# Kernel tuning notes

Measured on AMD Instinct MI355X. Metric: run time of the kernel, lower is better.

The kernel has to match this reference:

```python
import jax, jax.numpy as jnp
import numpy as np

B, N, T, CIN = 16, 400, 12, 2
HID, H, D = 256, 8, 32
P, EMB, TOPK, K = 3, 10, 16, 3


def _conv1d(x, w, b, dil):
    # x: (BN, C, T), w: (O, I, K); causal (left) padding like F.pad((pad,0))
    pad = (K - 1) * dil
    y = jax.lax.conv_general_dilated(x, w, (1,), [(pad, 0)], rhs_dilation=(dil,),
                                     dimension_numbers=('NCH', 'OIH', 'NCH'))
    return y + b[None, :, None]


def _ln(x, g, b):
    m = x.mean(-1, keepdims=True)
    v = x.var(-1, keepdims=True)
    return (x - m) / jnp.sqrt(v + 1e-5) * g + b


def setup_inputs() -> dict:
    key = jax.random.key(0)
    kit = iter(jax.random.split(key, 64))

    def g(shape, s=0.05):
        return jax.random.normal(next(kit), shape, jnp.float32) * s

    # fixed graph: ring with 8 neighbors + self loop -> L = 9*N edges
    idx = np.arange(N)
    offs = np.array([-4, -3, -2, -1, 0, 1, 2, 3, 4])
    recv = np.repeat(idx, offs.size)
    send = (recv + np.tile(offs, N)) % N
    L = recv.size

    inp = {
        'x': g((B, N, T, CIN), 1.0),
        'edge_feat': g((B, L, 2), 1.0),
        'fixed_edge_index': jnp.asarray(np.stack([recv, send]).astype(np.int32)),
        # GTCN layer 0 (dilation 1): gate/filter/skip convs + LayerNorm
        'wg0': g((HID, CIN, K)), 'bg0': jnp.zeros((HID,), jnp.float32),
        'wf0': g((HID, CIN, K)), 'bf0': jnp.zeros((HID,), jnp.float32),
        'ws0': g((HID, CIN, K)), 'bs0': jnp.zeros((HID,), jnp.float32),
        'ln0g': jnp.ones((HID,), jnp.float32), 'ln0b': jnp.zeros((HID,), jnp.float32),
        # GTCN layer 1 (dilation 2)
        'wg1': g((HID, HID, K)), 'bg1': jnp.zeros((HID,), jnp.float32),
        'wf1': g((HID, HID, K)), 'bf1': jnp.zeros((HID,), jnp.float32),
        'ws1': g((HID, HID, K)), 'bs1': jnp.zeros((HID,), jnp.float32),
        'ln1g': jnp.ones((HID,), jnp.float32), 'ln1b': jnp.zeros((HID,), jnp.float32),
        'wsk': g((CIN, HID)), 'bsk': jnp.zeros((HID,), jnp.float32),
        # sparse GAT on fixed physical graph (with 2-dim edge features)
        'sWq': g((HID, HID)), 'sWk': g((HID, HID)), 'sWv': g((HID, HID)),
        'sWe': g((2, HID)),
        'saq': g((H, D)), 'sak': g((H, D)), 'sae': g((H, D)),
        # dense GAT on adaptive adjacency
        'dWq': g((HID, HID)), 'dWk': g((HID, HID)), 'dWv': g((HID, HID)),
        'daq': g((H, D)), 'dak': g((H, D)),
        'E1': g((N, EMB), 0.5), 'E2': g((N, EMB), 0.5),
        # gated fusion
        'fW1': g((HID, HID)), 'fb1': jnp.zeros((HID,), jnp.float32),
        'fW2': g((HID, HID)), 'fb2': jnp.zeros((HID,), jnp.float32),
        'fW3': g((HID, HID)), 'fb3': jnp.zeros((HID,), jnp.float32),
        # prediction head
        'Wo': g((HID, P)), 'bo': jnp.zeros((P,), jnp.float32),
    }
    return inp


def reference(x, edge_feat,
              wg0, bg0, wf0, bf0, ws0, bs0, ln0g, ln0b,
              wg1, bg1, wf1, bf1, ws1, bs1, ln1g, ln1b, wsk, bsk,
              sWq, sWk, sWv, sWe, saq, sak, sae,
              dWq, dWk, dWv, daq, dak, E1, E2,
              fW1, fb1, fW2, fb2, fW3, fb3, Wo, bo,
              fixed_edge_index):
    Bb, Nn, Tt, _ = x.shape
    # ---- GTCN (gated temporal conv stack with residual skip) ----
    res = x @ wsk + bsk                                   # (B,N,T,HID)
    xc = x.reshape(Bb * Nn, Tt, -1).transpose(0, 2, 1)    # (BN,C,T)
    for (wg, bg, wf, bf, ws, bs, lg, lb), dil in (
            ((wg0, bg0, wf0, bf0, ws0, bs0, ln0g, ln0b), 1),
            ((wg1, bg1, wf1, bf1, ws1, bs1, ln1g, ln1b), 2)):
        gate = jax.nn.sigmoid(_conv1d(xc, wg, bg, dil))
        y = gate * _conv1d(xc, wf, bf, dil) + (1 - gate) * _conv1d(xc, ws, bs, dil)
        y = jax.nn.relu(_ln(y.transpose(0, 2, 1), lg, lb))  # (BN,T,HID)
        xc = y.transpose(0, 2, 1)
    h = xc.transpose(0, 2, 1).reshape(Bb, Nn, Tt, HID) + res
    hl = h[:, :, -1, :]                                   # (B,N,HID) last step

    # ---- sparse GAT on fixed physical graph (edge features) ----
    recv, send = fixed_edge_index[0], fixed_edge_index[1]
    q = (hl @ sWq).reshape(Bb, Nn, H, D)
    k = (hl @ sWk).reshape(Bb, Nn, H, D)
    v = (hl @ sWv).reshape(Bb, Nn, H, D)
    e = (edge_feat @ sWe).reshape(Bb, -1, H, D)
    s = (q[:, recv] * saq).sum(-1) + (k[:, send] * sak).sum(-1) + (e * sae).sum(-1)
    s = jax.nn.leaky_relu(s, 0.2)                         # (B,L,H)
    mx = jnp.full((Bb, Nn, H), -jnp.inf, s.dtype).at[:, recv].max(s)
    ex = jnp.exp(s - mx[:, recv])
    den = jnp.zeros((Bb, Nn, H), s.dtype).at[:, recv].add(ex)
    alpha = ex / jnp.clip(den[:, recv], 1e-12, None)
    agg = jnp.zeros((Bb, Nn, H, D), v.dtype).at[:, recv].add(alpha[..., None] * v[:, send])
    h_fixed = jax.nn.elu(agg.reshape(Bb, Nn, HID))

    # ---- dense GAT on adaptive (learned, top-k sparsified) adjacency ----
    A = jax.nn.softmax(jax.nn.relu(E1 @ E2.T), axis=-1)   # (N,N)
    kth = jax.lax.top_k(A, TOPK)[0][:, -1:]
    adj_adp = jnp.where(A >= kth, A, 0.0)
    q = (hl @ dWq).reshape(Bb, Nn, H, D)
    k = (hl @ dWk).reshape(Bb, Nn, H, D)
    v = (hl @ dWv).reshape(Bb, Nn, H, D)
    sc = (q * daq).sum(-1)[:, :, None, :] + (k * dak).sum(-1)[:, None, :, :]  # (B,N,N,H)
    sc = jax.nn.leaky_relu(sc, 0.2)
    sc = sc + jnp.log(jnp.clip(adj_adp, 1e-12, None))[None, :, :, None]      # log-adj trick
    sc = jnp.where((adj_adp > 0)[None, :, :, None], sc, -1e9)
    al = jax.nn.softmax(sc, axis=2)
    h_adp = jax.nn.elu(jnp.einsum('bnjh,bjhd->bnhd', al, v).reshape(Bb, Nn, HID))

    # ---- gated fusion + prediction head ----
    gate = jax.nn.sigmoid((h_fixed + h_adp) @ fW1 + fb1)
    fused = jnp.tanh(gate * (h_fixed @ fW2 + fb2) + (1 - gate) * (h_adp @ fW3 + fb3))
    return fused @ Wo + bo                                # (B,N,P)
```

## Files before the change

kernel.cpp:

```cpp
#include <hip/hip_runtime.h>
#include <math.h>

#define LL 3600
#define NODES 6400

typedef __attribute__((ext_vector_type(8))) _Float16 half8;
typedef __attribute__((ext_vector_type(4))) float f32x4;

__device__ __forceinline__ unsigned short f2h(float f) {
    union { _Float16 h; unsigned short u; } cv;
    cv.h = (_Float16)f;
    return cv.u;
}
__device__ __forceinline__ float h2f(unsigned short u) {
    union { unsigned short u; _Float16 h; } cv;
    cv.u = u;
    return (float)cv.h;
}

#define GLOAD16(gp, lp) __builtin_amdgcn_global_load_lds( \
    (const __attribute__((address_space(1))) unsigned int*)(const void*)(gp), \
    (__attribute__((address_space(3))) unsigned int*)(void*)(lp), 16, 0, 0)

__global__ __launch_bounds__(256) void prep_kernel(
    const float* __restrict__ wg1, const float* __restrict__ wf1, const float* __restrict__ ws1,
    const float* __restrict__ sWv, const float* __restrict__ dWv,
    const float* __restrict__ sWq, const float* __restrict__ saq,
    const float* __restrict__ sWk, const float* __restrict__ sak,
    const float* __restrict__ dWq, const float* __restrict__ daq,
    const float* __restrict__ dWk, const float* __restrict__ dak,
    const float* __restrict__ fW1, const float* __restrict__ fW2, const float* __restrict__ fW3,
    const float* __restrict__ sWe, const float* __restrict__ sae,
    const float* __restrict__ E1, const float* __restrict__ E2,
    const float* __restrict__ x,
    const float* __restrict__ wg0, const float* __restrict__ bg0,
    const float* __restrict__ wf0, const float* __restrict__ bf0,
    const float* __restrict__ ws0, const float* __restrict__ bs0,
    const float* __restrict__ lg0, const float* __restrict__ lb0,
    const float* __restrict__ bo,
    unsigned short* __restrict__ W1h,
    unsigned short* __restrict__ W2h,
    unsigned short* __restrict__ W3h,
    float* __restrict__ AeS,
    int* __restrict__ cnt, int* __restrict__ idxs, float* __restrict__ logv,
    unsigned short* __restrict__ Xh,
    float* __restrict__ out) {
    int bid = blockIdx.x;
    int tid = threadIdx.x;

    if (bid < 2304) {
        int idx = bid * 256 + tid;
        int n = idx / 768, k = idx % 768;
        int which = n >> 8, o = n & 255;
        int tt = k >> 8, i = k & 255;
        const float* w = which == 0 ? wg1 : (which == 1 ? wf1 : ws1);
        W1h[idx] = f2h(w[(o * 256 + i) * 3 + tt]);
    } else if (bid < 2944) {
        int idx = (bid - 2304) * 256 + tid;
        int n = idx / 256, k = idx % 256;
        float v = 0.f;
        if (n < 256) v = sWv[k * 256 + n];
        else if (n < 512) v = dWv[k * 256 + (n - 256)];
        else if (n < 544) {
            int j = n - 512, g = j >> 3, h = j & 7;
            const float* Wm = g == 0 ? sWq : (g == 1 ? sWk : (g == 2 ? dWq : dWk));
            const float* am = g == 0 ? saq : (g == 1 ? sak : (g == 2 ? daq : dak));
            float s = 0.f;
            for (int d = 0; d < 32; d++) s += Wm[k * 256 + h * 32 + d] * am[h * 32 + d];
            v = s;
        }
        W2h[idx] = f2h(v);
    } else if (bid < 4480) {
        int idx = (bid - 2944) * 256 + tid;
        int n = idx / 512, k = idx % 512;
        float v = 0.f;
        if (k < 256) {
            if (n < 256) v = fW1[k * 256 + n];
            else if (n < 512) v = fW2[k * 256 + (n - 256)];
        } else {
            int c = k - 256;
            if (n < 256) v = fW1[c * 256 + n];
            else if (n >= 512) v = fW3[c * 256 + (n - 512)];
        }
        W3h[idx] = f2h(v);
    } else if (bid == 4480) {
        if (tid < 16) {
            int cc = tid / 8, h = tid % 8;
            float s = 0.f;
            for (int d = 0; d < 32; d++) s += sWe[cc * 256 + h * 32 + d] * sae[h * 32 + d];
            AeS[tid] = s;
        }
    } else if (bid < 4581) {
        int n = ((bid - 4481) * 256 + tid) >> 6;
        int lane = tid & 63;
        if (n >= 400) return;
        float e1[10];
        #pragma unroll
        for (int k = 0; k < 10; k++) e1[k] = E1[n * 10 + k];
        float p[7];
        #pragma unroll
        for (int i = 0; i < 7; i++) {
            int j = i * 64 + lane;
            if (j < 400) {
                float s = 0.f;
                #pragma unroll
                for (int k = 0; k < 10; k++) s += e1[k] * E2[j * 10 + k];
                p[i] = fmaxf(s, 0.f);
            } else p[i] = -1e30f;
        }
        float mx = -1e30f;
        #pragma unroll
        for (int i = 0; i < 7; i++) mx = fmaxf(mx, p[i]);
        #pragma unroll
        for (int o = 32; o > 0; o >>= 1) mx = fmaxf(mx, __shfl_xor(mx, o, 64));
        float sum = 0.f;
        #pragma unroll
        for (int i = 0; i < 7; i++) {
            int j = i * 64 + lane;
            if (j < 400) { p[i] = expf(p[i] - mx); sum += p[i]; }
        }
        #pragma unroll
        for (int o = 32; o > 0; o >>= 1) sum += __shfl_xor(sum, o, 64);
        float inv = 1.f / sum;
        float m[7];
        #pragma unroll
        for (int i = 0; i < 7; i++) {
            int j = i * 64 + lane;
            if (j < 400) { p[i] *= inv; m[i] = p[i]; }
            else m[i] = -1e30f;
        }
        for (int it = 0; it < 15; ++it) {
            float lm = m[0];
            #pragma unroll
            for (int i = 1; i < 7; i++) lm = fmaxf(lm, m[i]);
            float gm = lm;
            #pragma unroll
            for (int o = 32; o > 0; o >>= 1) gm = fmaxf(gm, __shfl_xor(gm, o, 64));
            unsigned long long msk = __ballot(lm == gm);
            int first = (int)(__ffsll((long long)msk)) - 1;
            if (lane == first) {
                #pragma unroll
                for (int i = 0; i < 7; i++) {
                    if (m[i] == gm) { m[i] = -1e30f; break; }
                }
            }
        }
        float kth = m[0];
        #pragma unroll
        for (int i = 1; i < 7; i++) kth = fmaxf(kth, m[i]);
        #pragma unroll
        for (int o = 32; o > 0; o >>= 1) kth = fmaxf(kth, __shfl_xor(kth, o, 64));
        int base = 0;
        #pragma unroll
        for (int i = 0; i < 7; i++) {
            int j = i * 64 + lane;
            bool pred = (j < 400) && (p[i] >= kth);
            unsigned long long msk = __ballot(pred);
            int pre = __popcll(msk & ((lane == 63) ? 0x7fffffffffffffffull : ((1ull << lane) - 1)));
            if (pred) {
                int pos = base + pre;
                if (pos < 64) {
                    idxs[n * 64 + pos] = j;
                    logv[n * 64 + pos] = logf(fmaxf(p[i], 1e-12f));
                }
            }
            base += __popcll(msk);
        }
        if (lane == 0) cnt[n] = base < 64 ? base : 64;
    } else if (bid < 6181) {
        int lane = tid & 63;
        int node = (bid - 4581) * 4 + (tid >> 6);
        float xs[14];
        #pragma unroll
        for (int t = 0; t < 7; t++) {
            xs[t * 2]     = x[(size_t)(node * 12 + 5 + t) * 2];
            xs[t * 2 + 1] = x[(size_t)(node * 12 + 5 + t) * 2 + 1];
        }
        float wg[4][6], wf[4][6], wsv[4][6], bgv[4], bfv[4], bsv[4], gln[4], bln[4];
        #pragma unroll
        for (int cc = 0; cc < 4; cc++) {
            int o = lane * 4 + cc;
            #pragma unroll
            for (int i = 0; i < 6; i++) {
                wg[cc][i] = wg0[o * 6 + i];
                wf[cc][i] = wf0[o * 6 + i];
                wsv[cc][i] = ws0[o * 6 + i];
            }
            bgv[cc] = bg0[o]; bfv[cc] = bf0[o]; bsv[cc] = bs0[o];
            gln[cc] = lg0[o]; bln[cc] = lb0[o];
        }
        #pragma unroll
        for (int tt = 0; tt < 3; tt++) {
            int tb = 2 * tt;
            float y[4];
            float s1 = 0.f, s2 = 0.f;
            #pragma unroll
            for (int cc = 0; cc < 4; cc++) {
                float g = bgv[cc], f = bfv[cc], s = bsv[cc];
                #pragma unroll
                for (int k = 0; k < 3; k++) {
                    #pragma unroll
                    for (int c = 0; c < 2; c++) {
                        float xv = xs[(tb + k) * 2 + c];
                        g += wg[cc][c * 3 + k] * xv;
                        f += wf[cc][c * 3 + k] * xv;
                        s += wsv[cc][c * 3 + k] * xv;
                    }
                }
                float gate = 1.f / (1.f + expf(-g));
                y[cc] = gate * f + (1.f - gate) * s;
                s1 += y[cc];
                s2 += y[cc] * y[cc];
            }
            #pragma unroll
            for (int o = 32; o > 0; o >>= 1) {
                s1 += __shfl_xor(s1, o, 64);
                s2 += __shfl_xor(s2, o, 64);
            }
            float mean = s1 * (1.f / 256.f);
            float var = s2 * (1.f / 256.f) - mean * mean;
            float rstd = rsqrtf(var + 1e-5f);
            unsigned short h4[4];
            #pragma unroll
            for (int cc = 0; cc < 4; cc++) {
                float v = (y[cc] - mean) * rstd * gln[cc] + bln[cc];
                h4[cc] = f2h(fmaxf(v, 0.f));
            }
            unsigned long long pack = (unsigned long long)h4[0] | ((unsigned long long)h4[1] << 16)
                                    | ((unsigned long long)h4[2] << 32) | ((unsigned long long)h4[3] << 48);
            *(unsigned long long*)&Xh[(size_t)node * 768 + tt * 256 + lane * 4] = pack;
        }
    } else {
        int idx = (bid - 6181) * 256 + tid;
        if (idx < NODES * 3) out[idx] = bo[idx % 3];
    }
}

template<int K, int LDC, int GX>
__global__ __launch_bounds__(256, 6) void gemm_f16(
    const unsigned short* __restrict__ A,
    const unsigned short* __restrict__ BT,
    unsigned short* __restrict__ C) {
    __shared__ __align__(16) unsigned short lA[3][64 * 32];
    __shared__ __align__(16) unsigned short lB[3][64 * 32];
    int tid = threadIdx.x;
    int lane = tid & 63;
    int w = tid >> 6;
    int wm = w >> 1, wn = w & 1;
    int r = lane & 15, g4 = lane >> 4;

    constexpr int NWG = GX * 100;
    constexpr int Q = NWG / 8, R = NWG % 8;
    int flat = blockIdx.y * GX + blockIdx.x;
    int xcd = flat & 7, idx = flat >> 3;
    int nf = (xcd < R ? xcd * (Q + 1) : R * (Q + 1) + (xcd - R) * Q) + idx;
    int col0 = (nf % GX) * 64;
    int row0 = (nf / GX) * 64;

    f32x4 acc[2][2] = {};

    int rS = tid >> 2;
    int slot = tid & 3;
    int tk = (slot ^ (rS & 3)) * 8;

#define STAGE(sel, kk) do { \
    GLOAD16(A + (size_t)(row0 + rS) * K + (kk) + tk, &lA[sel][tid * 8]); \
    GLOAD16(BT + (size_t)(col0 + rS) * K + (kk) + tk, &lB[sel][tid * 8]); \
} while (0)

    int sw = (g4 ^ (r & 3)) << 3;

#define COMPUTE(cur) do { \
    half8 a_[2], b_[2]; \
    _Pragma("unroll") \
    for (int mi = 0; mi < 2; ++mi) \
        a_[mi] = *(const half8*)&lA[cur][(wm * 32 + mi * 16 + r) * 32 + sw]; \
    _Pragma("unroll") \
    for (int ni = 0; ni < 2; ++ni) \
        b_[ni] = *(const half8*)&lB[cur][(wn * 32 + ni * 16 + r) * 32 + sw]; \
    _Pragma("unroll") \
    for (int mi = 0; mi < 2; ++mi) \
        _Pragma("unroll") \
        for (int ni = 0; ni < 2; ++ni) \
            acc[mi][ni] = __builtin_amdgcn_mfma_f32_16x16x32_f16(a_[mi], b_[ni], acc[mi][ni], 0, 0, 0); \
} while (0)

    constexpr int NT = K >> 5;
    STAGE(0, 0);
    STAGE(1, 32);
    for (int t = 0; t < NT - 1; ++t) {
        asm volatile("s_waitcnt vmcnt(2)" ::: "memory");
        __builtin_amdgcn_s_barrier();
        if (t + 2 < NT) STAGE((t + 2) % 3, (t + 2) * 32);
        COMPUTE(t % 3);
    }
    asm volatile("s_waitcnt vmcnt(0)" ::: "memory");
    __builtin_amdgcn_s_barrier();
    COMPUTE((NT - 1) % 3);
#undef STAGE
#undef COMPUTE

    #pragma unroll
    for (int mi = 0; mi < 2; ++mi) {
        #pragma unroll
        for (int ni = 0; ni < 2; ++ni) {
            int rowb = row0 + wm * 32 + mi * 16 + g4 * 4;
            int colb = col0 + wn * 32 + ni * 16 + r;
            #pragma unroll
            for (int j = 0; j < 4; ++j)
                C[(size_t)(rowb + j) * LDC + colb] = f2h(acc[mi][ni][j]);
        }
    }
}

__global__ __launch_bounds__(256, 3) void gemm3_fused(
    const unsigned short* __restrict__ A,
    const unsigned short* __restrict__ BT,
    const float* __restrict__ fb1, const float* __restrict__ fb2, const float* __restrict__ fb3,
    const float* __restrict__ Wo,
    float* __restrict__ out) {
    __shared__ __align__(16) unsigned short lA[3][64 * 32];
    __shared__ __align__(16) unsigned short lB[3][3][64 * 32];
    int tid = threadIdx.x;
    int lane = tid & 63;
    int w = tid >> 6;
    int wm = w >> 1, wn = w & 1;
    int r = lane & 15, g4 = lane >> 4;

    constexpr int NWG = 400;
    constexpr int Q = NWG / 8;
    int flat = blockIdx.y * 4 + blockIdx.x;
    int xcd = flat & 7, idx = flat >> 3;
    int nf = xcd * Q + idx;
    int c0 = (nf % 4) * 64;
    int row0 = (nf / 4) * 64;

    f32x4 acc[3][2][2] = {};

    int rS = tid >> 2;
    int slot = tid & 3;
    int tk = (slot ^ (rS & 3)) * 8;

#define STAGE3(sel, kk) do { \
    GLOAD16(A + (size_t)(row0 + rS) * 512 + (kk) + tk, &lA[sel][tid * 8]); \
    GLOAD16(BT + (size_t)(c0 + rS) * 512 + (kk) + tk, &lB[sel][0][tid * 8]); \
    GLOAD16(BT + (size_t)(c0 + 256 + rS) * 512 + (kk) + tk, &lB[sel][1][tid * 8]); \
    GLOAD16(BT + (size_t)(c0 + 512 + rS) * 512 + (kk) + tk, &lB[sel][2][tid * 8]); \
} while (0)

    int sw = (g4 ^ (r & 3)) << 3;

#define COMPUTE3(cur) do { \
    half8 a_[2], b_[3][2]; \
    _Pragma("unroll") \
    for (int mi = 0; mi < 2; ++mi) \
        a_[mi] = *(const half8*)&lA[cur][(wm * 32 + mi * 16 + r) * 32 + sw]; \
    _Pragma("unroll") \
    for (int q = 0; q < 3; ++q) \
        _Pragma("unroll") \
        for (int ni = 0; ni < 2; ++ni) \
            b_[q][ni] = *(const half8*)&lB[cur][q][(wn * 32 + ni * 16 + r) * 32 + sw]; \
    _Pragma("unroll") \
    for (int q = 0; q < 3; ++q) \
        _Pragma("unroll") \
        for (int mi = 0; mi < 2; ++mi) \
            _Pragma("unroll") \
            for (int ni = 0; ni < 2; ++ni) \
                acc[q][mi][ni] = __builtin_amdgcn_mfma_f32_16x16x32_f16(a_[mi], b_[q][ni], acc[q][mi][ni], 0, 0, 0); \
} while (0)

    constexpr int NT = 16;
    STAGE3(0, 0);
    STAGE3(1, 32);
    for (int t = 0; t < NT - 1; ++t) {
        asm volatile("s_waitcnt vmcnt(4)" ::: "memory");
        __builtin_amdgcn_s_barrier();
        if (t + 2 < NT) STAGE3((t + 2) % 3, (t + 2) * 32);
        COMPUTE3(t % 3);
    }
    asm volatile("s_waitcnt vmcnt(0)" ::: "memory");
    __builtin_amdgcn_s_barrier();
    COMPUTE3((NT - 1) % 3);
#undef STAGE3
#undef COMPUTE3

    #pragma unroll
    for (int mi = 0; mi < 2; ++mi) {
        float v0[4] = {}, v1[4] = {}, v2[4] = {};
        #pragma unroll
        for (int ni = 0; ni < 2; ++ni) {
            int ch = c0 + wn * 32 + ni * 16 + r;
            float b1 = fb1[ch], b2 = fb2[ch], b3 = fb3[ch];
            float w0 = Wo[ch * 3 + 0], w1 = Wo[ch * 3 + 1], w2 = Wo[ch * 3 + 2];
            #pragma unroll
            for (int j = 0; j < 4; ++j) {
                float g = 1.f / (1.f + expf(-(acc[0][mi][ni][j] + b1)));
                float a2 = acc[1][mi][ni][j] + b2;
                float a3 = acc[2][mi][ni][j] + b3;
                float fused = tanhf(g * a2 + (1.f - g) * a3);
                v0[j] += fused * w0;
                v1[j] += fused * w1;
                v2[j] += fused * w2;
            }
        }
        #pragma unroll
        for (int off = 1; off < 16; off <<= 1) {
            #pragma unroll
            for (int j = 0; j < 4; ++j) {
                v0[j] += __shfl_xor(v0[j], off, 64);
                v1[j] += __shfl_xor(v1[j], off, 64);
                v2[j] += __shfl_xor(v2[j], off, 64);
            }
        }
        if (r == 0) {
            int rowb = row0 + wm * 32 + mi * 16 + g4 * 4;
            #pragma unroll
            for (int j = 0; j < 4; ++j) {
                atomicAdd(&out[(size_t)(rowb + j) * 3 + 0], v0[j]);
                atomicAdd(&out[(size_t)(rowb + j) * 3 + 1], v1[j]);
                atomicAdd(&out[(size_t)(rowb + j) * 3 + 2], v2[j]);
            }
        }
    }
}

__global__ __launch_bounds__(256) void epi1_kernel(
    const unsigned short* __restrict__ Y1, const float* __restrict__ x,
    const float* __restrict__ bg1, const float* __restrict__ bf1, const float* __restrict__ bs1,
    const float* __restrict__ lg, const float* __restrict__ lb,
    const float* __restrict__ wsk, const float* __restrict__ bsk,
    unsigned short* __restrict__ HLh) {
    int node = blockIdx.x, o = threadIdx.x;
    __shared__ float red[8];
    size_t base = (size_t)node * 768;
    float g = h2f(Y1[base + o]) + bg1[o];
    float f = h2f(Y1[base + 256 + o]) + bf1[o];
    float s = h2f(Y1[base + 512 + o]) + bs1[o];
    float gate = 1.f / (1.f + expf(-g));
    float y = gate * f + (1.f - gate) * s;
    float a = y, bb = y * y;
    #pragma unroll
    for (int off = 32; off > 0; off >>= 1) { a += __shfl_xor(a, off, 64); bb += __shfl_xor(bb, off, 64); }
    int w = o >> 6, l = o & 63;
    if (l == 0) { red[w] = a; red[4 + w] = bb; }
    __syncthreads();
    float sum = red[0] + red[1] + red[2] + red[3];
    float sq = red[4] + red[5] + red[6] + red[7];
    float mean = sum * (1.f / 256.f);
    float var = sq * (1.f / 256.f) - mean * mean;
    float v = (y - mean) * rsqrtf(var + 1e-5f) * lg[o] + lb[o];
    v = fmaxf(v, 0.f);
    float x0 = x[(size_t)(node * 12 + 11) * 2];
    float x1 = x[(size_t)(node * 12 + 11) * 2 + 1];
    float res = x0 * wsk[o] + x1 * wsk[256 + o] + bsk[o];
    HLh[(size_t)node * 256 + o] = f2h(v + res);
}

__global__ __launch_bounds__(256) void gat_kernel(
    const unsigned short* __restrict__ Y2, const float* __restrict__ ef,
    const int* __restrict__ fei, const float* __restrict__ AeS,
    const int* __restrict__ cnt, const int* __restrict__ idxs, const float* __restrict__ logv,
    unsigned short* __restrict__ Uh) {
    int node = blockIdx.x;
    int b = node / 400, n = node % 400;
    int tid = threadIdx.x;
    __shared__ int snd[9];
    __shared__ float alf[9][8];
    __shared__ float invdf[8];
    __shared__ int jidx[64];
    __shared__ float sca[64][8];
    __shared__ float alb[64][8];
    __shared__ float invda[8];
    __shared__ float svf[9][8];
    int c = cnt[n];

    if (tid < 64) {
        int lane = tid;
        if (lane < 9) snd[lane] = fei[LL + n * 9 + lane];
        for (int e = lane; e < 72; e += 64) {
            int j = e >> 3, h = e & 7;
            int l = n * 9 + j;
            float e0 = ef[((size_t)b * LL + l) * 2];
            float e1 = ef[((size_t)b * LL + l) * 2 + 1];
            float ae = e0 * AeS[h] + e1 * AeS[8 + h];
            float aq = h2f(Y2[(size_t)node * 640 + 512 + h]);
            float ak = h2f(Y2[((size_t)(b * 400 + snd[j])) * 640 + 520 + h]);
            float s = aq + ak + ae;
            svf[j][h] = s > 0.f ? s : 0.2f * s;
        }
        if (lane < 8) {
            int h = lane;
            float mx = -1e30f;
            #pragma unroll
            for (int j = 0; j < 9; j++) mx = fmaxf(mx, svf[j][h]);
            float den = 0.f;
            #pragma unroll
            for (int j = 0; j < 9; j++) { float e = expf(svf[j][h] - mx); alf[j][h] = e; den += e; }
            invdf[h] = 1.f / fmaxf(den, 1e-12f);
        }
    } else if (tid < 128) {
        int lane = tid - 64;
        if (lane < c) jidx[lane] = idxs[n * 64 + lane];
        float jl = (lane < c) ? logv[n * 64 + lane] : 0.f;
        for (int e = lane; e < c * 8; e += 64) {
            int j = e >> 3, h = e & 7;
            float aq = h2f(Y2[(size_t)node * 640 + 528 + h]);
            float ak = h2f(Y2[((size_t)(b * 400 + jidx[j])) * 640 + 536 + h]);
            float s = aq + ak;
            s = s > 0.f ? s : 0.2f * s;
            sca[j][h] = s + __shfl(jl, j, 64);
        }
        int h = lane >> 3, grp = lane & 7;
        float mx = -1e30f;
        for (int j = grp; j < c; j += 8) mx = fmaxf(mx, sca[j][h]);
        #pragma unroll
        for (int o = 1; o < 8; o <<= 1) mx = fmaxf(mx, __shfl_xor(mx, o, 64));
        float s = 0.f;
        for (int j = grp; j < c; j += 8) { float e = expf(sca[j][h] - mx); alb[j][h] = e; s += e; }
        #pragma unroll
        for (int o = 1; o < 8; o <<= 1) s += __shfl_xor(s, o, 64);
        if (grp == 0) invda[h] = 1.f / s;
    }
    __syncthreads();

    if (tid < 128) {
        int ch = tid * 2;
        int h = ch >> 5;
        float a0 = 0.f, a1 = 0.f;
        #pragma unroll
        for (int j = 0; j < 9; j++) {
            unsigned v = *(const unsigned*)&Y2[((size_t)(b * 400 + snd[j])) * 640 + ch];
            float al = alf[j][h];
            a0 += al * h2f((unsigned short)(v & 0xffff));
            a1 += al * h2f((unsigned short)(v >> 16));
        }
        float iv = invdf[h];
        a0 *= iv; a1 *= iv;
        a0 = a0 > 0.f ? a0 : (expf(a0) - 1.f);
        a1 = a1 > 0.f ? a1 : (expf(a1) - 1.f);
        unsigned o = (unsigned)f2h(a0) | ((unsigned)f2h(a1) << 16);
        *(unsigned*)&Uh[(size_t)node * 512 + ch] = o;
    } else {
        int ch = (tid - 128) * 2;
        int h = ch >> 5;
        float a0 = 0.f, a1 = 0.f;
        for (int j = 0; j < c; j++) {
            unsigned v = *(const unsigned*)&Y2[((size_t)(b * 400 + jidx[j])) * 640 + 256 + ch];
            float al = alb[j][h];
            a0 += al * h2f((unsigned short)(v & 0xffff));
            a1 += al * h2f((unsigned short)(v >> 16));
        }
        float iv = invda[h];
        a0 *= iv; a1 *= iv;
        a0 = a0 > 0.f ? a0 : (expf(a0) - 1.f);
        a1 = a1 > 0.f ? a1 : (expf(a1) - 1.f);
        unsigned o = (unsigned)f2h(a0) | ((unsigned)f2h(a1) << 16);
        *(unsigned*)&Uh[(size_t)node * 512 + 256 + ch] = o;
    }
}

extern "C" void kernel_launch(void* const* d_in, const int* in_sizes, int n_in,
                              void* d_out, int out_size, void* d_ws, size_t ws_size,
                              hipStream_t stream) {
    const float* x   = (const float*)d_in[0];
    const float* ef  = (const float*)d_in[1];
    const int*   fei = (const int*)d_in[2];
    const float* wg0 = (const float*)d_in[3];
    const float* bg0 = (const float*)d_in[4];
    const float* wf0 = (const float*)d_in[5];
    const float* bf0 = (const float*)d_in[6];
    const float* ws0 = (const float*)d_in[7];
    const float* bs0 = (const float*)d_in[8];
    const float* ln0g = (const float*)d_in[9];
    const float* ln0b = (const float*)d_in[10];
    const float* wg1 = (const float*)d_in[11];
    const float* bg1 = (const float*)d_in[12];
    const float* wf1 = (const float*)d_in[13];
    const float* bf1 = (const float*)d_in[14];
    const float* ws1 = (const float*)d_in[15];
    const float* bs1 = (const float*)d_in[16];
    const float* ln1g = (const float*)d_in[17];
    const float* ln1b = (const float*)d_in[18];
    const float* wsk = (const float*)d_in[19];
    const float* bsk = (const float*)d_in[20];
    const float* sWq = (const float*)d_in[21];
    const float* sWk = (const float*)d_in[22];
    const float* sWv = (const float*)d_in[23];
    const float* sWe = (const float*)d_in[24];
    const float* saq = (const float*)d_in[25];
    const float* sak = (const float*)d_in[26];
    const float* sae = (const float*)d_in[27];
    const float* dWq = (const float*)d_in[28];
    const float* dWk = (const float*)d_in[29];
    const float* dWv = (const float*)d_in[30];
    const float* daq = (const float*)d_in[31];
    const float* dak = (const float*)d_in[32];
    const float* E1  = (const float*)d_in[33];
    const float* E2  = (const float*)d_in[34];
    const float* fW1 = (const float*)d_in[35];
    const float* fb1 = (const float*)d_in[36];
    const float* fW2 = (const float*)d_in[37];
    const float* fb2 = (const float*)d_in[38];
    const float* fW3 = (const float*)d_in[39];
    const float* fb3 = (const float*)d_in[40];
    const float* Wo  = (const float*)d_in[41];
    const float* bo  = (const float*)d_in[42];
    float* out = (float*)d_out;

    char* b = (char*)d_ws;
    unsigned short* Xh  = (unsigned short*)(b + 0);
    unsigned short* Yh  = (unsigned short*)(b + 9830400);
    unsigned short* HLh = (unsigned short*)(b + 19660800);
    unsigned short* Uh  = (unsigned short*)(b + 22937600);
    unsigned short* W1h = (unsigned short*)(b + 29491200);
    unsigned short* W2h = (unsigned short*)(b + 30670848);
    unsigned short* W3h = (unsigned short*)(b + 30998528);
    float*          AES = (float*)(b + 31784960);
    float*          LOGV= (float*)(b + 31785216);
    int*            CNT = (int*)(b + 31887616);
    int*            IDX = (int*)(b + 31889216);

    prep_kernel<<<6256, 256, 0, stream>>>(
        wg1, wf1, ws1,
        sWv, dWv, sWq, saq, sWk, sak, dWq, daq, dWk, dak,
        fW1, fW2, fW3, sWe, sae, E1, E2,
        x, wg0, bg0, wf0, bf0, ws0, bs0, ln0g, ln0b, bo,
        W1h, W2h, W3h, AES,
        CNT, IDX, LOGV, Xh, out);

    gemm_f16<768, 768, 12><<<dim3(12, 100), 256, 0, stream>>>(Xh, W1h, Yh);

    epi1_kernel<<<NODES, 256, 0, stream>>>(Yh, x, bg1, bf1, bs1, ln1g, ln1b, wsk, bsk, HLh);

    gemm_f16<256, 640, 9><<<dim3(9, 100), 256, 0, stream>>>(HLh, W2h, Yh);

    gat_kernel<<<NODES, 256, 0, stream>>>(Yh, ef, fei, AES, CNT, IDX, LOGV, Uh);

    gemm3_fused<<<dim3(4, 100), 256, 0, stream>>>(Uh, W3h, fb1, fb2, fb3, Wo, out);
}
```

Baseline: 99.09 us.

## Halve gemm3 row tile to double grid; process one node per wave in epi1

The fused final GEMM now uses 32-row tiles instead of 64, which doubles the workgroup count to 800 for better CU occupancy. The B staging loads are redistributed across all threads, and only the upper half of the threads stage A, so the per-wave vmcnt waits differ. The first epilogue kernel now handles one node per 64-lane wave with 4 channels per lane, using vector loads/stores and no shared-memory reduction or block barrier. The trade-off is that B tiles are reloaded twice as often and more atomics hit the output.

```diff
diff --git a/kernel.cpp b/kernel.cpp
--- a/kernel.cpp
+++ b/kernel.cpp
@@ -6,6 +6,7 @@
 
 typedef __attribute__((ext_vector_type(8))) _Float16 half8;
 typedef __attribute__((ext_vector_type(4))) float f32x4;
+typedef __attribute__((ext_vector_type(4))) unsigned short ushort4v;
 
 __device__ __forceinline__ unsigned short f2h(float f) {
     union { _Float16 h; unsigned short u; } cv;
@@ -319,7 +320,7 @@
     const float* __restrict__ fb1, const float* __restrict__ fb2, const float* __restrict__ fb3,
     const float* __restrict__ Wo,
     float* __restrict__ out) {
-    __shared__ __align__(16) unsigned short lA[3][64 * 32];
+    __shared__ __align__(16) unsigned short lA[3][32 * 32];
     __shared__ __align__(16) unsigned short lB[3][3][64 * 32];
     int tid = threadIdx.x;
     int lane = tid & 63;
@@ -327,34 +328,36 @@
     int wm = w >> 1, wn = w & 1;
     int r = lane & 15, g4 = lane >> 4;
 
-    constexpr int NWG = 400;
-    constexpr int Q = NWG / 8;
     int flat = blockIdx.y * 4 + blockIdx.x;
     int xcd = flat & 7, idx = flat >> 3;
-    int nf = xcd * Q + idx;
+    int nf = xcd * 100 + idx;
     int c0 = (nf % 4) * 64;
-    int row0 = (nf / 4) * 64;
-
-    f32x4 acc[3][2][2] = {};
-
-    int rS = tid >> 2;
-    int slot = tid & 3;
-    int tk = (slot ^ (rS & 3)) * 8;
+    int row0 = (nf / 4) * 32;
+
+    f32x4 acc[3][2] = {};
+
+    int aTid = tid - 128;
+    int aRow = aTid >> 2, aSlot = aTid & 3;
+    int aTk = (aSlot ^ (aRow & 3)) * 8;
 
 #define STAGE3(sel, kk) do { \
-    GLOAD16(A + (size_t)(row0 + rS) * 512 + (kk) + tk, &lA[sel][tid * 8]); \
-    GLOAD16(BT + (size_t)(c0 + rS) * 512 + (kk) + tk, &lB[sel][0][tid * 8]); \
-    GLOAD16(BT + (size_t)(c0 + 256 + rS) * 512 + (kk) + tk, &lB[sel][1][tid * 8]); \
-    GLOAD16(BT + (size_t)(c0 + 512 + rS) * 512 + (kk) + tk, &lB[sel][2][tid * 8]); \
+    _Pragma("unroll") \
+    for (int q = 0; q < 3; ++q) { \
+        int cch = q * 256 + tid; \
+        int brow = cch >> 2, bslot = cch & 3; \
+        int q2 = brow >> 6, r2 = brow & 63; \
+        int btk = (bslot ^ (r2 & 3)) * 8; \
+        GLOAD16(BT + (size_t)(c0 + q2 * 256 + r2) * 512 + (kk) + btk, &lB[sel][0][cch * 8]); \
+    } \
+    if (tid >= 128) \
+        GLOAD16(A + (size_t)(row0 + aRow) * 512 + (kk) + aTk, &lA[sel][aTid * 8]); \
 } while (0)
 
     int sw = (g4 ^ (r & 3)) << 3;
 
 #define COMPUTE3(cur) do { \
-    half8 a_[2], b_[3][2]; \
-    _Pragma("unroll") \
-    for (int mi = 0; mi < 2; ++mi) \
-        a_[mi] = *(const half8*)&lA[cur][(wm * 32 + mi * 16 + r) * 32 + sw]; \
+    half8 a_, b_[3][2]; \
+    a_ = *(const half8*)&lA[cur][(wm * 16 + r) * 32 + sw]; \
     _Pragma("unroll") \
     for (int q = 0; q < 3; ++q) \
         _Pragma("unroll") \
@@ -363,17 +366,16 @@
     _Pragma("unroll") \
     for (int q = 0; q < 3; ++q) \
         _Pragma("unroll") \
-        for (int mi = 0; mi < 2; ++mi) \
-            _Pragma("unroll") \
-            for (int ni = 0; ni < 2; ++ni) \
-                acc[q][mi][ni] = __builtin_amdgcn_mfma_f32_16x16x32_f16(a_[mi], b_[q][ni], acc[q][mi][ni], 0, 0, 0); \
+        for (int ni = 0; ni < 2; ++ni) \
+            acc[q][ni] = __builtin_amdgcn_mfma_f32_16x16x32_f16(a_, b_[q][ni], acc[q][ni], 0, 0, 0); \
 } while (0)
 
     constexpr int NT = 16;
     STAGE3(0, 0);
     STAGE3(1, 32);
     for (int t = 0; t < NT - 1; ++t) {
-        asm volatile("s_waitcnt vmcnt(4)" ::: "memory");
+        if (w < 2) { asm volatile("s_waitcnt vmcnt(3)" ::: "memory"); }
+        else       { asm volatile("s_waitcnt vmcnt(4)" ::: "memory"); }
         __builtin_amdgcn_s_barrier();
         if (t + 2 < NT) STAGE3((t + 2) % 3, (t + 2) * 32);
         COMPUTE3(t % 3);
@@ -384,42 +386,39 @@
 #undef STAGE3
 #undef COMPUTE3
 
+    float v0[4] = {}, v1[4] = {}, v2[4] = {};
     #pragma unroll
-    for (int mi = 0; mi < 2; ++mi) {
-        float v0[4] = {}, v1[4] = {}, v2[4] = {};
-        #pragma unroll
-        for (int ni = 0; ni < 2; ++ni) {
-            int ch = c0 + wn * 32 + ni * 16 + r;
-            float b1 = fb1[ch], b2 = fb2[ch], b3 = fb3[ch];
-            float w0 = Wo[ch * 3 + 0], w1 = Wo[ch * 3 + 1], w2 = Wo[ch * 3 + 2];
-            #pragma unroll
-            for (int j = 0; j < 4; ++j) {
-                float g = 1.f / (1.f + expf(-(acc[0][mi][ni][j] + b1)));
-                float a2 = acc[1][mi][ni][j] + b2;
-                float a3 = acc[2][mi][ni][j] + b3;
-                float fused = tanhf(g * a2 + (1.f - g) * a3);
-                v0[j] += fused * w0;
-                v1[j] += fused * w1;
-                v2[j] += fused * w2;
-            }
-        }
-        #pragma unroll
-        for (int off = 1; off < 16; off <<= 1) {
-            #pragma unroll
-            for (int j = 0; j < 4; ++j) {
-                v0[j] += __shfl_xor(v0[j], off, 64);
-                v1[j] += __shfl_xor(v1[j], off, 64);
-                v2[j] += __shfl_xor(v2[j], off, 64);
-            }
-        }
-        if (r == 0) {
-            int rowb = row0 + wm * 32 + mi * 16 + g4 * 4;
-            #pragma unroll
-            for (int j = 0; j < 4; ++j) {
-                atomicAdd(&out[(size_t)(rowb + j) * 3 + 0], v0[j]);
-                atomicAdd(&out[(size_t)(rowb + j) * 3 + 1], v1[j]);
-                atomicAdd(&out[(size_t)(rowb + j) * 3 + 2], v2[j]);
-            }
+    for (int ni = 0; ni < 2; ++ni) {
+        int ch = c0 + wn * 32 + ni * 16 + r;
+        float b1 = fb1[ch], b2 = fb2[ch], b3 = fb3[ch];
+        float w0 = Wo[ch * 3 + 0], w1 = Wo[ch * 3 + 1], w2 = Wo[ch * 3 + 2];
+        #pragma unroll
+        for (int j = 0; j < 4; ++j) {
+            float g = 1.f / (1.f + expf(-(acc[0][ni][j] + b1)));
+            float a2 = acc[1][ni][j] + b2;
+            float a3 = acc[2][ni][j] + b3;
+            float fused = tanhf(g * a2 + (1.f - g) * a3);
+            v0[j] += fused * w0;
+            v1[j] += fused * w1;
+            v2[j] += fused * w2;
+        }
+    }
+    #pragma unroll
+    for (int off = 1; off < 16; off <<= 1) {
+        #pragma unroll
+        for (int j = 0; j < 4; ++j) {
+            v0[j] += __shfl_xor(v0[j], off, 64);
+            v1[j] += __shfl_xor(v1[j], off, 64);
+            v2[j] += __shfl_xor(v2[j], off, 64);
+        }
+    }
+    if (r == 0) {
+        int rowb = row0 + wm * 16 + g4 * 4;
+        #pragma unroll
+        for (int j = 0; j < 4; ++j) {
+            atomicAdd(&out[(size_t)(rowb + j) * 3 + 0], v0[j]);
+            atomicAdd(&out[(size_t)(rowb + j) * 3 + 1], v1[j]);
+            atomicAdd(&out[(size_t)(rowb + j) * 3 + 2], v2[j]);
         }
     }
 }
@@ -430,30 +429,47 @@
     const float* __restrict__ lg, const float* __restrict__ lb,
     const float* __restrict__ wsk, const float* __restrict__ bsk,
     unsigned short* __restrict__ HLh) {
-    int node = blockIdx.x, o = threadIdx.x;
-    __shared__ float red[8];
+    int lane = threadIdx.x & 63;
+    int node = blockIdx.x * 4 + (threadIdx.x >> 6);
     size_t base = (size_t)node * 768;
-    float g = h2f(Y1[base + o]) + bg1[o];
-    float f = h2f(Y1[base + 256 + o]) + bf1[o];
-    float s = h2f(Y1[base + 512 + o]) + bs1[o];
-    float gate = 1.f / (1.f + expf(-g));
-    float y = gate * f + (1.f - gate) * s;
-    float a = y, bb = y * y;
+    ushort4v yg = *(const ushort4v*)&Y1[base + lane * 4];
+    ushort4v yf = *(const ushort4v*)&Y1[base + 256 + lane * 4];
+    ushort4v ys = *(const ushort4v*)&Y1[base + 512 + lane * 4];
+    float y[4];
+    float s1 = 0.f, s2 = 0.f;
     #pragma unroll
-    for (int off = 32; off > 0; off >>= 1) { a += __shfl_xor(a, off, 64); bb += __shfl_xor(bb, off, 64); }
-    int w = o >> 6, l = o & 63;
-    if (l == 0) { red[w] = a; red[4 + w] = bb; }
-    __syncthreads();
-    float sum = red[0] + red[1] + red[2] + red[3];
-    float sq = red[4] + red[5] + red[6] + red[7];
-    float mean = sum * (1.f / 256.f);
-    float var = sq * (1.f / 256.f) - mean * mean;
-    float v = (y - mean) * rsqrtf(var + 1e-5f) * lg[o] + lb[o];
-    v = fmaxf(v, 0.f);
+    for (int cc = 0; cc < 4; cc++) {
+        int o = lane * 4 + cc;
+        float g = h2f(yg[cc]) + bg1[o];
+        float f = h2f(yf[cc]) + bf1[o];
+        float s = h2f(ys[cc]) + bs1[o];
+        float gate = 1.f / (1.f + expf(-g));
+        y[cc] = gate * f + (1.f - gate) * s;
+        s1 += y[cc];
+        s2 += y[cc] * y[cc];
+    }
+    #pragma unroll
+    for (int off = 32; off > 0; off >>= 1) {
+        s1 += __shfl_xor(s1, off, 64);
+        s2 += __shfl_xor(s2, off, 64);
+    }
+    float mean = s1 * (1.f / 256.f);
+    float var = s2 * (1.f / 256.f) - mean * mean;
+    float rstd = rsqrtf(var + 1e-5f);
     float x0 = x[(size_t)(node * 12 + 11) * 2];
     float x1 = x[(size_t)(node * 12 + 11) * 2 + 1];
-    float res = x0 * wsk[o] + x1 * wsk[256 + o] + bsk[o];
-    HLh[(size_t)node * 256 + o] = f2h(v + res);
+    unsigned short h4[4];
+    #pragma unroll
+    for (int cc = 0; cc < 4; cc++) {
+        int o = lane * 4 + cc;
+        float v = (y[cc] - mean) * rstd * lg[o] + lb[o];
+        v = fmaxf(v, 0.f);
+        float res = x0 * wsk[o] + x1 * wsk[256 + o] + bsk[o];
+        h4[cc] = f2h(v + res);
+    }
+    unsigned long long pack = (unsigned long long)h4[0] | ((unsigned long long)h4[1] << 16)
+                            | ((unsigned long long)h4[2] << 32) | ((unsigned long long)h4[3] << 48);
+    *(unsigned long long*)&HLh[(size_t)node * 256 + lane * 4] = pack;
 }
 
 __global__ __launch_bounds__(256) void gat_kernel(
@@ -630,11 +646,11 @@
 
     gemm_f16<768, 768, 12><<<dim3(12, 100), 256, 0, stream>>>(Xh, W1h, Yh);
 
-    epi1_kernel<<<NODES, 256, 0, stream>>>(Yh, x, bg1, bf1, bs1, ln1g, ln1b, wsk, bsk, HLh);
+    epi1_kernel<<<1600, 256, 0, stream>>>(Yh, x, bg1, bf1, bs1, ln1g, ln1b, wsk, bsk, HLh);
 
     gemm_f16<256, 640, 9><<<dim3(9, 100), 256, 0, stream>>>(HLh, W2h, Yh);
 
     gat_kernel<<<NODES, 256, 0, stream>>>(Yh, ef, fei, AES, CNT, IDX, LOGV, Uh);
 
-    gemm3_fused<<<dim3(4, 100), 256, 0, stream>>>(Uh, W3h, fb1, fb2, fb3, Wo, out);
-}
+    gemm3_fused<<<dim3(4, 200), 256, 0, stream>>>(Uh, W3h, fb1, fb2, fb3, Wo, out);
+}
```

Measured after the change: 103.8 us. +4.8%, slower.
